# Performance work log

Measured on AMD Instinct MI355X. Metric: run time of the kernel, lower is better.

Reference implementation:

```python
import jax, jax.numpy as jnp
import numpy as np

CAT_SIZES = [31360, 6807, 18, 94]
TOTAL = int(sum(CAT_SIZES))          # 38279
EMB = 128
N_FIELDS = len(CAT_SIZES)
D_IN = N_FIELDS * EMB                # 512 (num_features is empty)
MLP_DIMS = [2048, 1024, 512]
B = 16384
OFFSETS = np.concatenate([[0], np.cumsum(CAT_SIZES)[:-1]]).astype(np.int32)


def setup_inputs() -> dict:
    key = jax.random.key(0)
    ks = jax.random.split(key, 20)
    # x holds raw per-field category ids stored as float32 (as the torch model expects)
    cols = [jax.random.randint(ks[i], (B,), 0, s) for i, s in enumerate(CAT_SIZES)]
    x = jnp.stack(cols, axis=1).astype(jnp.float32)

    bias = jnp.zeros((1,), jnp.float32)
    fc = jax.random.uniform(ks[4], (TOTAL, 1), dtype=jnp.float32)          # nn.Parameter(torch.rand)
    emb_table = jax.random.normal(ks[5], (TOTAL, EMB), dtype=jnp.float32)  # nn.Embedding default N(0,1)

    dims = [D_IN] + MLP_DIMS + [1]
    params = {}
    for i in range(len(dims) - 1):
        fan_in = dims[i]
        bound = 1.0 / np.sqrt(fan_in)
        params[f"W{i+1}"] = jax.random.uniform(ks[6 + 2 * i], (dims[i], dims[i + 1]), jnp.float32, -bound, bound)
        params[f"b{i+1}"] = jax.random.uniform(ks[7 + 2 * i], (dims[i + 1],), jnp.float32, -bound, bound)

    return dict(x=x, bias=bias, fc=fc, emb_table=emb_table, **params)


def reference(x, bias, fc, emb_table, W1, b1, W2, b2, W3, b3, W4, b4):
    cat = x.astype(jnp.int32)                       # [B, F] raw per-field ids
    b = cat.shape[0]

    # embedding lookup with RAW (un-offset) ids, faithful to the original code
    embed_x = emb_table[cat].reshape(b, -1)          # [B, F*EMB]

    # one_hot(offset ids) @ fc  ==  sum_f fc[offset ids]  (offset ranges disjoint)
    gidx = cat + jnp.asarray(OFFSETS)                # [B, F] global ids
    lin = jnp.sum(fc[gidx, 0], axis=1)               # [B]
    fm_y = bias + lin                                # [B]

    # FM term: embed_x is 2-D, so sum over dim=1 collapses features;
    # the keepdim sum over dim=-1 then collapses the BATCH dim to shape (1,)
    # (a quirk of the original code that we reproduce exactly)
    square_of_sum = jnp.sum(embed_x, axis=1) ** 2    # [B]
    sum_of_square = jnp.sum(embed_x ** 2, axis=1)    # [B]
    fm_y = fm_y + 0.5 * jnp.sum(square_of_sum - sum_of_square, axis=-1, keepdims=True)  # [B]
    fm_y = fm_y[:, None]                             # [B,1]

    # MLP (eval mode: dropout is identity)
    h = embed_x
    for W, bb in ((W1, b1), (W2, b2), (W3, b3)):
        h = jax.nn.relu(h @ W + bb)
    mlp_y = h @ W4 + b4                              # [B,1]

    return jax.nn.sigmoid(fm_y + mlp_y)              # [B,1]
```

## Files before the change

kernel.cpp:

```cpp
#include <hip/hip_runtime.h>
#include <hip/hip_fp8.h>
#include <cstdint>


typedef float f32x4 __attribute__((ext_vector_type(4)));
typedef int i32x4 __attribute__((ext_vector_type(4)));
typedef int i32x8 __attribute__((ext_vector_type(8)));

#define GLOAD16(gptr, lptr)                                                \
  __builtin_amdgcn_global_load_lds(                                        \
      (const __attribute__((address_space(1))) void*)(gptr),               \
      (__attribute__((address_space(3))) void*)(lptr), 16, 0, 0)

__device__ inline uint32_t f2fp4(float v) {
  uint32_t s = (__float_as_uint(v) >> 31) << 3;
  float a = fabsf(v);
  uint32_t m;
  if (a < 0.25f) m = 0;
  else if (a < 0.75f) m = 1;
  else if (a < 1.25f) m = 2;
  else if (a < 1.75f) m = 3;
  else if (a < 2.5f)  m = 4;
  else if (a < 3.5f)  m = 5;
  else if (a < 5.0f)  m = 6;
  else m = 7;
  return s | m;
}

static constexpr size_t OFF_LIN  = 0;
static constexpr size_t OFF_PART = 65536;
static constexpr size_t OFF_ACC  = 98304;
static constexpr size_t OFF_EMB  = 262144;
static constexpr size_t OFF_H1   = OFF_EMB + 8388608ull;
static constexpr size_t OFF_H2   = OFF_H1 + 33554432ull;
static constexpr size_t OFF_W1T  = OFF_H2 + 16777216ull;
static constexpr size_t OFF_W2T  = OFF_W1T + 524288ull;
static constexpr size_t OFF_W3T  = OFF_W2T + 1048576ull;

__global__ void prep(const float* __restrict__ W1, const float* __restrict__ W2,
                     const float* __restrict__ W3, uint8_t* __restrict__ W1T,
                     uint8_t* __restrict__ W2T, uint8_t* __restrict__ W3T,
                     const float* __restrict__ x, const float* __restrict__ fc,
                     const float* __restrict__ emb, uint8_t* __restrict__ ebf,
                     float* __restrict__ lin, float* __restrict__ partials,
                     float* __restrict__ dotacc) {
  __shared__ __align__(16) float smem[32 * 33];
  int blk = blockIdx.x;
  int tid = threadIdx.x;
  if (blk < 3584) {
    const float* W;
    uint8_t* WT;
    int K, N, bx, by;
    if (blk < 1024) {
      W = W1; WT = W1T; K = 512; N = 2048; bx = blk & 63; by = blk >> 6;
    } else if (blk < 3072) {
      int t = blk - 1024;
      W = W2; WT = W2T; K = 2048; N = 1024; bx = t & 31; by = t >> 5;
    } else {
      int t = blk - 3072;
      W = W3; WT = W3T; K = 1024; N = 512; bx = t & 15; by = t >> 4;
    }
    int tx = tid & 31, ty = tid >> 5;
    int n0 = bx * 32, k0 = by * 32;
#pragma unroll
    for (int i = ty; i < 32; i += 8)
      smem[i * 33 + tx] = W[(size_t)(k0 + i) * N + n0 + tx];
    __syncthreads();
    if (tx < 16) {
#pragma unroll
      for (int i = ty; i < 32; i += 8) {
        uint32_t lo = f2fp4(smem[(2 * tx) * 33 + i] * 128.f);
        uint32_t hi = f2fp4(smem[(2 * tx + 1) * 33 + i] * 128.f);
        WT[(size_t)(n0 + i) * (K >> 1) + (k0 >> 1) + tx] =
            (uint8_t)(lo | (hi << 4));
      }
    }
  } else if (blk < 7680) {
    int gb = blk - 3584;
    int wv = tid >> 6, lane = tid & 63;
    int b = gb * 4 + wv;
    int f = lane >> 4;
    int idx = (int)x[b * 4 + f];
    const float* row = emb + (size_t)idx * 128 + (lane & 15) * 8;
    float4 v0 = ((const float4*)row)[0];
    float4 v1 = ((const float4*)row)[1];
    float s = v0.x + v0.y + v0.z + v0.w + v1.x + v1.y + v1.z + v1.w;
    float q = v0.x * v0.x + v0.y * v0.y + v0.z * v0.z + v0.w * v0.w +
              v1.x * v1.x + v1.y * v1.y + v1.z * v1.z + v1.w * v1.w;

    int lo = 0, hi = 0;
    lo = __builtin_amdgcn_cvt_pk_fp8_f32(v0.x, v0.y, lo, false);
    lo = __builtin_amdgcn_cvt_pk_fp8_f32(v0.z, v0.w, lo, true);
    hi = __builtin_amdgcn_cvt_pk_fp8_f32(v1.x, v1.y, hi, false);
    hi = __builtin_amdgcn_cvt_pk_fp8_f32(v1.z, v1.w, hi, true);
    int2 pk = make_int2(lo, hi);
    *(int2*)(ebf + (size_t)b * 512 + lane * 8) = pk;

    float lp = 0.f;
    if ((lane & 15) == 0) {
      int off = (f == 1) ? 31360 : (f == 2) ? 38167 : (f == 3) ? 38185 : 0;
      lp = fc[idx + off];
    }
#pragma unroll
    for (int m = 32; m; m >>= 1) {
      s += __shfl_xor(s, m);
      q += __shfl_xor(q, m);
      lp += __shfl_xor(lp, m);
    }
    float* pt = smem;
    if (lane == 0) {
      lin[b] = lp;
      pt[wv] = s * s - q;
    }
    __syncthreads();
    if (tid == 0) partials[gb] = pt[0] + pt[1] + pt[2] + pt[3];
  } else {
    int zb = blk - 7680;
    ((float4*)dotacc)[zb * 256 + tid] = make_float4(0.f, 0.f, 0.f, 0.f);
  }
}

__global__ __launch_bounds__(256, 2) void gemm_mx_relu(
    const uint8_t* __restrict__ A, const uint8_t* __restrict__ BT,
    const float* __restrict__ bias, uint8_t* __restrict__ C, int K, int N,
    int GX) {
  __shared__ __align__(16) uint8_t As[128][256];
  __shared__ __align__(16) uint8_t Bs[256][128];
  int bid = blockIdx.x;
  int by = (bid & 7) + ((bid >> 3) / GX) * 8;
  int bx = (bid >> 3) & (GX - 1);
  int tid = threadIdx.x;
  int wv = tid >> 6, lane = tid & 63;
  int m0 = by * 128, n0 = bx * 256;
  int mw = (wv >> 1) * 64, nw = (wv & 1) * 128;
  int ml = lane & 15, kg = lane >> 4;
  int Kb2 = K >> 1;

  int arow = wv * 4 + (lane >> 4);
  int acol = ((lane & 15) ^ arow) * 16;
  int brow = wv * 8 + (lane >> 3);
  int bcol = ((lane & 7) ^ (brow & 7)) * 16;

  f32x4 acc[4][8];
#pragma unroll
  for (int i = 0; i < 4; ++i)
#pragma unroll
    for (int j = 0; j < 8; ++j) acc[i][j] = (f32x4){0.f, 0.f, 0.f, 0.f};

  for (int kt = 0; kt < K; kt += 256) {
#pragma unroll
    for (int r = 0; r < 8; ++r) {
      const uint8_t* ga = A + (size_t)(m0 + r * 16 + arow) * K + kt + acol;
      GLOAD16(ga, &As[r * 16 + wv * 4][0]);
    }
#pragma unroll
    for (int r = 0; r < 8; ++r) {
      const uint8_t* gb =
          BT + (size_t)(n0 + r * 32 + brow) * Kb2 + (kt >> 1) + bcol;
      GLOAD16(gb, &Bs[r * 32 + wv * 8][0]);
    }
    __syncthreads();

    i32x4 z = (i32x4){0, 0, 0, 0};
#pragma unroll
    for (int j = 0; j < 2; ++j) {
      int pa0 = ((8 * j + 2 * kg) ^ ml) * 16;
      int pa1 = ((8 * j + 2 * kg + 1) ^ ml) * 16;
      int pb = ((4 * j + kg) ^ (ml & 7)) * 16;
      i32x8 af[4];
#pragma unroll
      for (int mt = 0; mt < 4; ++mt) {
        int ra = mw + mt * 16 + ml;
        i32x4 a0 = *(const i32x4*)&As[ra][pa0];
        i32x4 a1 = *(const i32x4*)&As[ra][pa1];
        af[mt] = __builtin_shufflevector(a0, a1, 0, 1, 2, 3, 4, 5, 6, 7);
      }
#pragma unroll
      for (int nt = 0; nt < 8; ++nt) {
        i32x4 vb = *(const i32x4*)&Bs[nw + nt * 16 + ml][pb];
        i32x8 bf = __builtin_shufflevector(vb, z, 0, 1, 2, 3, 4, 5, 6, 7);
#pragma unroll
        for (int mt = 0; mt < 4; ++mt)
          acc[mt][nt] = __builtin_amdgcn_mfma_scale_f32_16x16x128_f8f6f4(
              af[mt], bf, acc[mt][nt],
               0,  4,
              0, 0x7F7F7F7F, 0, 0x78787878);
      }
    }
    __syncthreads();
  }

  int rbase = kg * 4;
#pragma unroll
  for (int nt = 0; nt < 8; ++nt) {
    int col = n0 + nw + nt * 16 + ml;
    float bv = bias[col];
#pragma unroll
    for (int mt = 0; mt < 4; ++mt) {
      int row = m0 + mw + mt * 16 + rbase;
      float v0 = acc[mt][nt][0] + bv, v1 = acc[mt][nt][1] + bv;
      float v2 = acc[mt][nt][2] + bv, v3 = acc[mt][nt][3] + bv;
      v0 = v0 > 0.f ? v0 : 0.f;
      v1 = v1 > 0.f ? v1 : 0.f;
      v2 = v2 > 0.f ? v2 : 0.f;
      v3 = v3 > 0.f ? v3 : 0.f;
      int w01 = __builtin_amdgcn_cvt_pk_fp8_f32(v0, v1, 0, false);
      int w23 = __builtin_amdgcn_cvt_pk_fp8_f32(v2, v3, 0, false);
      C[(size_t)(row + 0) * N + col] = (uint8_t)(w01 & 0xFF);
      C[(size_t)(row + 1) * N + col] = (uint8_t)((w01 >> 8) & 0xFF);
      C[(size_t)(row + 2) * N + col] = (uint8_t)(w23 & 0xFF);
      C[(size_t)(row + 3) * N + col] = (uint8_t)((w23 >> 8) & 0xFF);
    }
  }
}

__global__ __launch_bounds__(256, 2) void gemm_mx_dot(
    const uint8_t* __restrict__ A, const uint8_t* __restrict__ BT,
    const float* __restrict__ bias, const float* __restrict__ W4,
    float* __restrict__ dotacc, int K, int N, int GX) {
  __shared__ __align__(16) uint8_t As[128][256];
  __shared__ __align__(16) uint8_t Bs[256][128];
  int bid = blockIdx.x;
  int by = (bid & 7) + ((bid >> 3) / GX) * 8;
  int bx = (bid >> 3) & (GX - 1);
  int tid = threadIdx.x;
  int wv = tid >> 6, lane = tid & 63;
  int m0 = by * 128, n0 = bx * 256;
  int mw = (wv >> 1) * 64, nw = (wv & 1) * 128;
  int ml = lane & 15, kg = lane >> 4;
  int Kb2 = K >> 1;

  int arow = wv * 4 + (lane >> 4);
  int acol = ((lane & 15) ^ arow) * 16;
  int brow = wv * 8 + (lane >> 3);
  int bcol = ((lane & 7) ^ (brow & 7)) * 16;

  f32x4 acc[4][8];
#pragma unroll
  for (int i = 0; i < 4; ++i)
#pragma unroll
    for (int j = 0; j < 8; ++j) acc[i][j] = (f32x4){0.f, 0.f, 0.f, 0.f};

  for (int kt = 0; kt < K; kt += 256) {
#pragma unroll
    for (int r = 0; r < 8; ++r) {
      const uint8_t* ga = A + (size_t)(m0 + r * 16 + arow) * K + kt + acol;
      GLOAD16(ga, &As[r * 16 + wv * 4][0]);
    }
#pragma unroll
    for (int r = 0; r < 8; ++r) {
      const uint8_t* gb =
          BT + (size_t)(n0 + r * 32 + brow) * Kb2 + (kt >> 1) + bcol;
      GLOAD16(gb, &Bs[r * 32 + wv * 8][0]);
    }
    __syncthreads();

    i32x4 z = (i32x4){0, 0, 0, 0};
#pragma unroll
    for (int j = 0; j < 2; ++j) {
      int pa0 = ((8 * j + 2 * kg) ^ ml) * 16;
      int pa1 = ((8 * j + 2 * kg + 1) ^ ml) * 16;
      int pb = ((4 * j + kg) ^ (ml & 7)) * 16;
      i32x8 af[4];
#pragma unroll
      for (int mt = 0; mt < 4; ++mt) {
        int ra = mw + mt * 16 + ml;
        i32x4 a0 = *(const i32x4*)&As[ra][pa0];
        i32x4 a1 = *(const i32x4*)&As[ra][pa1];
        af[mt] = __builtin_shufflevector(a0, a1, 0, 1, 2, 3, 4, 5, 6, 7);
      }
#pragma unroll
      for (int nt = 0; nt < 8; ++nt) {
        i32x4 vb = *(const i32x4*)&Bs[nw + nt * 16 + ml][pb];
        i32x8 bf = __builtin_shufflevector(vb, z, 0, 1, 2, 3, 4, 5, 6, 7);
#pragma unroll
        for (int mt = 0; mt < 4; ++mt)
          acc[mt][nt] = __builtin_amdgcn_mfma_scale_f32_16x16x128_f8f6f4(
              af[mt], bf, acc[mt][nt],
              0, 4, 0, 0x7F7F7F7F, 0, 0x78787878);
      }
    }
    __syncthreads();
  }

  float bv[8], w4v[8];
#pragma unroll
  for (int nt = 0; nt < 8; ++nt) {
    int col = n0 + nw + nt * 16 + ml;
    bv[nt] = bias[col];
    w4v[nt] = W4[col];
  }
  int rbase = kg * 4;
#pragma unroll
  for (int mt = 0; mt < 4; ++mt) {
#pragma unroll
    for (int r = 0; r < 4; ++r) {
      float p = 0.f;
#pragma unroll
      for (int nt = 0; nt < 8; ++nt) {
        float v = acc[mt][nt][r] + bv[nt];
        v = v > 0.f ? v : 0.f;
        p += v * w4v[nt];
      }
#pragma unroll
      for (int m = 1; m < 16; m <<= 1) p += __shfl_xor(p, m);
      if (ml == 0)
        atomicAdd(&dotacc[m0 + mw + mt * 16 + rbase + r], p);
    }
  }
}

__global__ void final_out(const float* __restrict__ part,
                          const float* __restrict__ dotacc,
                          const float* __restrict__ lin,
                          const float* __restrict__ bias,
                          const float* __restrict__ b4,
                          float* __restrict__ out) {
  __shared__ float ps[4];
  int tid = threadIdx.x;
  float v = 0.f;
  for (int i = tid; i < 4096; i += 256) v += part[i];
#pragma unroll
  for (int m = 32; m; m >>= 1) v += __shfl_xor(v, m);
  if ((tid & 63) == 0) ps[tid >> 6] = v;
  __syncthreads();
  float S = ps[0] + ps[1] + ps[2] + ps[3];
  int i = blockIdx.x * 256 + tid;
  float z = dotacc[i] + b4[0] + bias[0] + lin[i] + 0.5f * S;
  out[i] = 1.f / (1.f + expf(-z));
}

extern "C" void kernel_launch(void* const* d_in, const int* in_sizes, int n_in,
                              void* d_out, int out_size, void* d_ws,
                              size_t ws_size, hipStream_t stream) {
  const float* x    = (const float*)d_in[0];
  const float* bias = (const float*)d_in[1];
  const float* fc   = (const float*)d_in[2];
  const float* emb  = (const float*)d_in[3];
  const float* W1   = (const float*)d_in[4];
  const float* b1   = (const float*)d_in[5];
  const float* W2   = (const float*)d_in[6];
  const float* b2   = (const float*)d_in[7];
  const float* W3   = (const float*)d_in[8];
  const float* b3   = (const float*)d_in[9];
  const float* W4   = (const float*)d_in[10];
  const float* b4   = (const float*)d_in[11];
  float* out = (float*)d_out;

  char* ws = (char*)d_ws;
  float* lin    = (float*)(ws + OFF_LIN);
  float* part   = (float*)(ws + OFF_PART);
  float* dacc   = (float*)(ws + OFF_ACC);
  uint8_t* EMBb = (uint8_t*)(ws + OFF_EMB);
  uint8_t* H1   = (uint8_t*)(ws + OFF_H1);
  uint8_t* H2   = (uint8_t*)(ws + OFF_H2);
  uint8_t* W1T  = (uint8_t*)(ws + OFF_W1T);
  uint8_t* W2T  = (uint8_t*)(ws + OFF_W2T);
  uint8_t* W3T  = (uint8_t*)(ws + OFF_W3T);

  prep<<<7696, 256, 0, stream>>>(W1, W2, W3, W1T, W2T, W3T, x, fc, emb, EMBb,
                                 lin, part, dacc);

  gemm_mx_relu<<<1024, 256, 0, stream>>>(EMBb, W1T, b1, H1, 512, 2048, 8);
  gemm_mx_relu<<<512, 256, 0, stream>>>(H1, W2T, b2, H2, 2048, 1024, 4);
  gemm_mx_dot<<<256, 256, 0, stream>>>(H2, W3T, b3, W4, dacc, 1024, 512, 2);

  final_out<<<64, 256, 0, stream>>>(part, dacc, lin, bias, b4, out);
}
```

Before: 174.1 us.

## Store hidden activations as scaled FP4 and run FP4xFP4 MFMA in later layers

Hidden activations H1 and H2 are now quantized to packed FP4 (E2M1) with per-layer output scaling instead of FP8. Layers 2 and 3 therefore load half as many A bytes and issue FP4xFP4 scaled MFMAs. The weight transpose permutes K packing for W2/W3 so it matches the new activation nibble layout. This cuts activation memory traffic and LDS footprint, at the cost of much coarser activation precision, which may hurt accuracy.

Measured after the change: 165.7 us, median of 2. 1.05x faster.

```diff
diff --git a/kernel.cpp b/kernel.cpp
--- a/kernel.cpp
+++ b/kernel.cpp
@@ -25,6 +25,15 @@
   else if (a < 5.0f)  m = 6;
   else m = 7;
   return s | m;
+}
+
+__device__ inline uint32_t enc4(float x) {
+  float c = fminf(fmaxf(x, 0.5f), 6.0f);
+  uint32_t u = __float_as_uint(c);
+  u += 0x001FFFFFu + ((u >> 22) & 1u);
+  int code = (int)(u >> 22) - 252;
+  code = code < 1 ? 1 : code;
+  return x < 0.25f ? 0u : (uint32_t)code;
 }
 
 static constexpr size_t OFF_LIN  = 0;
@@ -51,14 +60,18 @@
     const float* W;
     uint8_t* WT;
     int K, N, bx, by;
+    bool perm;
     if (blk < 1024) {
       W = W1; WT = W1T; K = 512; N = 2048; bx = blk & 63; by = blk >> 6;
+      perm = false;
     } else if (blk < 3072) {
       int t = blk - 1024;
       W = W2; WT = W2T; K = 2048; N = 1024; bx = t & 31; by = t >> 5;
+      perm = true;
     } else {
       int t = blk - 3072;
       W = W3; WT = W3T; K = 1024; N = 512; bx = t & 15; by = t >> 4;
+      perm = true;
     }
     int tx = tid & 31, ty = tid >> 5;
     int n0 = bx * 32, k0 = by * 32;
@@ -67,10 +80,12 @@
       smem[i * 33 + tx] = W[(size_t)(k0 + i) * N + n0 + tx];
     __syncthreads();
     if (tx < 16) {
+      int kA = perm ? tx : 2 * tx;
+      int kB = perm ? tx + 16 : 2 * tx + 1;
 #pragma unroll
       for (int i = ty; i < 32; i += 8) {
-        uint32_t lo = f2fp4(smem[(2 * tx) * 33 + i] * 128.f);
-        uint32_t hi = f2fp4(smem[(2 * tx + 1) * 33 + i] * 128.f);
+        uint32_t lo = f2fp4(smem[kA * 33 + i] * 128.f);
+        uint32_t hi = f2fp4(smem[kB * 33 + i] * 128.f);
         WT[(size_t)(n0 + i) * (K >> 1) + (k0 >> 1) + tx] =
             (uint8_t)(lo | (hi << 4));
       }
@@ -120,11 +135,13 @@
   }
 }
 
-__global__ __launch_bounds__(256, 2) void gemm_mx_relu(
+template <bool AFP4>
+__global__ __launch_bounds__(256, 2) void gemm_mx_q4(
     const uint8_t* __restrict__ A, const uint8_t* __restrict__ BT,
     const float* __restrict__ bias, uint8_t* __restrict__ C, int K, int N,
-    int GX) {
-  __shared__ __align__(16) uint8_t As[128][256];
+    int GX, int sa, float osc) {
+  constexpr int ABYTES = AFP4 ? 128 : 256;
+  __shared__ __align__(16) uint8_t As[128][ABYTES];
   __shared__ __align__(16) uint8_t Bs[256][128];
   int bid = blockIdx.x;
   int by = (bid & 7) + ((bid >> 3) / GX) * 8;
@@ -136,8 +153,10 @@
   int ml = lane & 15, kg = lane >> 4;
   int Kb2 = K >> 1;
 
-  int arow = wv * 4 + (lane >> 4);
-  int acol = ((lane & 15) ^ arow) * 16;
+  int arow16 = wv * 4 + (lane >> 4);
+  int acol16 = ((lane & 15) ^ arow16) * 16;
+  int arow8 = lane >> 3;
+  int acol8 = ((lane & 7) ^ arow8) * 16;
   int brow = wv * 8 + (lane >> 3);
   int bcol = ((lane & 7) ^ (brow & 7)) * 16;
 
@@ -148,10 +167,20 @@
     for (int j = 0; j < 8; ++j) acc[i][j] = (f32x4){0.f, 0.f, 0.f, 0.f};
 
   for (int kt = 0; kt < K; kt += 256) {
-#pragma unroll
-    for (int r = 0; r < 8; ++r) {
-      const uint8_t* ga = A + (size_t)(m0 + r * 16 + arow) * K + kt + acol;
-      GLOAD16(ga, &As[r * 16 + wv * 4][0]);
+    if constexpr (!AFP4) {
+#pragma unroll
+      for (int r = 0; r < 8; ++r) {
+        const uint8_t* ga = A + (size_t)(m0 + r * 16 + arow16) * K + kt + acol16;
+        GLOAD16(ga, &As[r * 16 + wv * 4][0]);
+      }
+    } else {
+#pragma unroll
+      for (int r = 0; r < 4; ++r) {
+        int g = r * 4 + wv;
+        const uint8_t* ga =
+            A + (size_t)(m0 + 8 * g + arow8) * Kb2 + (kt >> 1) + acol8;
+        GLOAD16(ga, &As[8 * g][0]);
+      }
     }
 #pragma unroll
     for (int r = 0; r < 8; ++r) {
@@ -164,16 +193,22 @@
     i32x4 z = (i32x4){0, 0, 0, 0};
 #pragma unroll
     for (int j = 0; j < 2; ++j) {
-      int pa0 = ((8 * j + 2 * kg) ^ ml) * 16;
-      int pa1 = ((8 * j + 2 * kg + 1) ^ ml) * 16;
       int pb = ((4 * j + kg) ^ (ml & 7)) * 16;
       i32x8 af[4];
 #pragma unroll
       for (int mt = 0; mt < 4; ++mt) {
         int ra = mw + mt * 16 + ml;
-        i32x4 a0 = *(const i32x4*)&As[ra][pa0];
-        i32x4 a1 = *(const i32x4*)&As[ra][pa1];
-        af[mt] = __builtin_shufflevector(a0, a1, 0, 1, 2, 3, 4, 5, 6, 7);
+        if constexpr (!AFP4) {
+          int pa0 = ((8 * j + 2 * kg) ^ ml) * 16;
+          int pa1 = ((8 * j + 2 * kg + 1) ^ ml) * 16;
+          i32x4 a0 = *(const i32x4*)&As[ra][pa0];
+          i32x4 a1 = *(const i32x4*)&As[ra][pa1];
+          af[mt] = __builtin_shufflevector(a0, a1, 0, 1, 2, 3, 4, 5, 6, 7);
+        } else {
+          int pa = ((4 * j + kg) ^ (ml & 7)) * 16;
+          i32x4 a0 = *(const i32x4*)&As[ra][pa];
+          af[mt] = __builtin_shufflevector(a0, z, 0, 1, 2, 3, 4, 5, 6, 7);
+        }
       }
 #pragma unroll
       for (int nt = 0; nt < 8; ++nt) {
@@ -183,33 +218,31 @@
         for (int mt = 0; mt < 4; ++mt)
           acc[mt][nt] = __builtin_amdgcn_mfma_scale_f32_16x16x128_f8f6f4(
               af[mt], bf, acc[mt][nt],
-               0,  4,
-              0, 0x7F7F7F7F, 0, 0x78787878);
+               AFP4 ? 4 : 0,  4,
+              0, sa, 0, 0x78787878);
       }
     }
     __syncthreads();
   }
 
   int rbase = kg * 4;
-#pragma unroll
-  for (int nt = 0; nt < 8; ++nt) {
-    int col = n0 + nw + nt * 16 + ml;
-    float bv = bias[col];
-#pragma unroll
-    for (int mt = 0; mt < 4; ++mt) {
-      int row = m0 + mw + mt * 16 + rbase;
-      float v0 = acc[mt][nt][0] + bv, v1 = acc[mt][nt][1] + bv;
-      float v2 = acc[mt][nt][2] + bv, v3 = acc[mt][nt][3] + bv;
-      v0 = v0 > 0.f ? v0 : 0.f;
-      v1 = v1 > 0.f ? v1 : 0.f;
-      v2 = v2 > 0.f ? v2 : 0.f;
-      v3 = v3 > 0.f ? v3 : 0.f;
-      int w01 = __builtin_amdgcn_cvt_pk_fp8_f32(v0, v1, 0, false);
-      int w23 = __builtin_amdgcn_cvt_pk_fp8_f32(v2, v3, 0, false);
-      C[(size_t)(row + 0) * N + col] = (uint8_t)(w01 & 0xFF);
-      C[(size_t)(row + 1) * N + col] = (uint8_t)((w01 >> 8) & 0xFF);
-      C[(size_t)(row + 2) * N + col] = (uint8_t)(w23 & 0xFF);
-      C[(size_t)(row + 3) * N + col] = (uint8_t)((w23 >> 8) & 0xFF);
+  int NB = N >> 1;
+  int cb0 = ((n0 + nw) >> 1) + ml;
+  float bvo[8];
+#pragma unroll
+  for (int nt = 0; nt < 8; ++nt) bvo[nt] = bias[n0 + nw + nt * 16 + ml] * osc;
+#pragma unroll
+  for (int mt = 0; mt < 4; ++mt) {
+    int row = m0 + mw + mt * 16 + rbase;
+#pragma unroll
+    for (int p = 0; p < 4; ++p) {
+#pragma unroll
+      for (int r = 0; r < 4; ++r) {
+        float xl = fmaxf(fmaf(acc[mt][2 * p][r], osc, bvo[2 * p]), 0.f);
+        float xh = fmaxf(fmaf(acc[mt][2 * p + 1][r], osc, bvo[2 * p + 1]), 0.f);
+        C[(size_t)(row + r) * NB + cb0 + p * 16] =
+            (uint8_t)(enc4(xl) | (enc4(xh) << 4));
+      }
     }
   }
 }
@@ -217,8 +250,8 @@
 __global__ __launch_bounds__(256, 2) void gemm_mx_dot(
     const uint8_t* __restrict__ A, const uint8_t* __restrict__ BT,
     const float* __restrict__ bias, const float* __restrict__ W4,
-    float* __restrict__ dotacc, int K, int N, int GX) {
-  __shared__ __align__(16) uint8_t As[128][256];
+    float* __restrict__ dotacc, int K, int N, int GX, int sa) {
+  __shared__ __align__(16) uint8_t As[128][128];
   __shared__ __align__(16) uint8_t Bs[256][128];
   int bid = blockIdx.x;
   int by = (bid & 7) + ((bid >> 3) / GX) * 8;
@@ -230,8 +263,8 @@
   int ml = lane & 15, kg = lane >> 4;
   int Kb2 = K >> 1;
 
-  int arow = wv * 4 + (lane >> 4);
-  int acol = ((lane & 15) ^ arow) * 16;
+  int arow8 = lane >> 3;
+  int acol8 = ((lane & 7) ^ arow8) * 16;
   int brow = wv * 8 + (lane >> 3);
   int bcol = ((lane & 7) ^ (brow & 7)) * 16;
 
@@ -243,9 +276,11 @@
 
   for (int kt = 0; kt < K; kt += 256) {
 #pragma unroll
-    for (int r = 0; r < 8; ++r) {
-      const uint8_t* ga = A + (size_t)(m0 + r * 16 + arow) * K + kt + acol;
-      GLOAD16(ga, &As[r * 16 + wv * 4][0]);
+    for (int r = 0; r < 4; ++r) {
+      int g = r * 4 + wv;
+      const uint8_t* ga =
+          A + (size_t)(m0 + 8 * g + arow8) * Kb2 + (kt >> 1) + acol8;
+      GLOAD16(ga, &As[8 * g][0]);
     }
 #pragma unroll
     for (int r = 0; r < 8; ++r) {
@@ -258,16 +293,14 @@
     i32x4 z = (i32x4){0, 0, 0, 0};
 #pragma unroll
     for (int j = 0; j < 2; ++j) {
-      int pa0 = ((8 * j + 2 * kg) ^ ml) * 16;
-      int pa1 = ((8 * j + 2 * kg + 1) ^ ml) * 16;
       int pb = ((4 * j + kg) ^ (ml & 7)) * 16;
       i32x8 af[4];
 #pragma unroll
       for (int mt = 0; mt < 4; ++mt) {
         int ra = mw + mt * 16 + ml;
-        i32x4 a0 = *(const i32x4*)&As[ra][pa0];
-        i32x4 a1 = *(const i32x4*)&As[ra][pa1];
-        af[mt] = __builtin_shufflevector(a0, a1, 0, 1, 2, 3, 4, 5, 6, 7);
+        int pa = ((4 * j + kg) ^ (ml & 7)) * 16;
+        i32x4 a0 = *(const i32x4*)&As[ra][pa];
+        af[mt] = __builtin_shufflevector(a0, z, 0, 1, 2, 3, 4, 5, 6, 7);
       }
 #pragma unroll
       for (int nt = 0; nt < 8; ++nt) {
@@ -277,7 +310,8 @@
         for (int mt = 0; mt < 4; ++mt)
           acc[mt][nt] = __builtin_amdgcn_mfma_scale_f32_16x16x128_f8f6f4(
               af[mt], bf, acc[mt][nt],
-              0, 4, 0, 0x7F7F7F7F, 0, 0x78787878);
+               4,  4,
+              0, sa, 0, 0x78787878);
       }
     }
     __syncthreads();
@@ -361,9 +395,12 @@
   prep<<<7696, 256, 0, stream>>>(W1, W2, W3, W1T, W2T, W3T, x, fc, emb, EMBb,
                                  lin, part, dacc);
 
-  gemm_mx_relu<<<1024, 256, 0, stream>>>(EMBb, W1T, b1, H1, 512, 2048, 8);
-  gemm_mx_relu<<<512, 256, 0, stream>>>(H1, W2T, b2, H2, 2048, 1024, 4);
-  gemm_mx_dot<<<256, 256, 0, stream>>>(H2, W3T, b3, W4, dacc, 1024, 512, 2);
+  gemm_mx_q4<false><<<1024, 256, 0, stream>>>(EMBb, W1T, b1, H1, 512, 2048, 8,
+                                              0x7F7F7F7F, 2.0f);
+  gemm_mx_q4<true><<<512, 256, 0, stream>>>(H1, W2T, b2, H2, 2048, 1024, 4,
+                                            0x7E7E7E7E, 4.0f);
+  gemm_mx_dot<<<256, 256, 0, stream>>>(H2, W3T, b3, W4, dacc, 1024, 512, 2,
+                                       0x7D7D7D7D);
 
   final_out<<<64, 256, 0, stream>>>(part, dacc, lin, bias, b4, out);
 }
```
